# Kernel optimization log

Measured on AMD Instinct MI355X. Metric: run time of the kernel, lower is better.

## Reference

```python
import jax, jax.numpy as jnp
import numpy as np

EPS = 1e-6
STRIDES = (8, 16, 32)
IOU_THR = 0.5
GAMMA = 2.0
ALPHA = 1.0


def _ciou(b1, b2):
    # b1, b2: [..., 4] xywh boxes (broadcastable). Returns CIOU [...].
    b1xy, b1wh = b1[..., :2], b1[..., 2:]
    b2xy, b2wh = b2[..., :2], b2[..., 2:]
    b1lt, b1rb = b1xy - b1wh * 0.5, b1xy + b1wh * 0.5
    b2lt, b2rb = b2xy - b2wh * 0.5, b2xy + b2wh * 0.5
    lo1, hi1 = jnp.minimum(b1lt, b1rb), jnp.maximum(b1lt, b1rb)
    lo2, hi2 = jnp.minimum(b2lt, b2rb), jnp.maximum(b2lt, b2rb)
    area1 = (hi1[..., 0] - lo1[..., 0]) * (hi1[..., 1] - lo1[..., 1])
    area2 = (hi2[..., 0] - lo2[..., 0]) * (hi2[..., 1] - lo2[..., 1])
    iwh = jnp.clip(jnp.minimum(hi1, hi2) - jnp.maximum(lo1, lo2), 0.0, None)
    inter = iwh[..., 0] * iwh[..., 1]
    union = area1 + area2 - inter
    ious = inter / jnp.maximum(union, EPS)
    # smallest enclosing box diagonal
    owh = jnp.maximum(hi1, hi2) - jnp.minimum(lo1, lo2)
    c2 = jnp.maximum(owh[..., 0] ** 2 + owh[..., 1] ** 2, EPS)
    rho2 = jnp.sum((b1xy - b2xy) ** 2, axis=-1)
    u = rho2 / c2
    v = (4.0 / (np.pi ** 2)) * (
        jnp.arctan(b2wh[..., 0] / jnp.maximum(b2wh[..., 1], EPS))
        - jnp.arctan(b1wh[..., 0] / jnp.maximum(b1wh[..., 1], EPS))
    ) ** 2
    alpha = v / jnp.maximum(1.0 - ious + v, EPS)
    return ious - (u + alpha * v)


def _bce_logits(x, t):
    # stable BCEWithLogits, reduction='none'
    return jnp.logaddexp(0.0, x) - x * t


def _focal(x, t):
    return _bce_logits(x, t) * ALPHA * jnp.abs(t - jax.nn.sigmoid(x)) ** GAMMA


def _layer_loss(p, p_d, label, bboxes, stride):
    bs, grid = p.shape[0], p.shape[1]
    img_size = float(stride * grid)
    p_conf = p[..., 4:5]
    p_cls = p[..., 5:]
    p_d_xywh = p_d[..., :4]
    label_xywh = label[..., :4]
    obj = label[..., 4:5]
    mix = label[..., 5:6]
    label_cls = label[..., 6:]

    ciou = _ciou(p_d_xywh, label_xywh)[..., None]
    scale = 2.0 - label_xywh[..., 2:3] * label_xywh[..., 3:4] / (img_size ** 2)
    loss_ciou = obj * scale * (1.0 - ciou) * mix

    # pairwise CIOU between every pred box and up to 150 GT boxes: [bs,g,g,A,150]
    iou = _ciou(p_d_xywh[..., None, :], bboxes[:, None, None, None, :, :])
    iou_max = jnp.max(iou, axis=-1, keepdims=True)
    noobj = (1.0 - obj) * (iou_max < IOU_THR).astype(p.dtype)

    focal = _focal(p_conf, obj)
    loss_conf = (obj * focal + noobj * focal) * mix
    loss_cls = obj * _bce_logits(p_cls, label_cls) * mix

    l_ciou = jnp.sum(loss_ciou) / bs
    l_conf = jnp.sum(loss_conf) / bs
    l_cls = jnp.sum(loss_cls) / bs
    return l_ciou, l_conf, l_cls


def setup_inputs() -> dict:
    key = jax.random.key(0)
    B, A, NC, IMG = 4, 3, 20, 608
    grids = [76, 38, 19]
    inp = {}
    for i, g in enumerate(grids):
        k = jax.random.fold_in(key, i)
        ks = jax.random.split(k, 10)
        inp[f"p{i}"] = jax.random.normal(ks[0], (B, g, g, A, 5 + NC), jnp.float32)
        # decoded predictions: positive xywh in image coords + raw conf/cls
        xy = jax.random.uniform(ks[1], (B, g, g, A, 2)) * IMG
        wh = jax.random.uniform(ks[2], (B, g, g, A, 2)) * 120.0 + 2.0
        cc = jax.random.normal(ks[3], (B, g, g, A, 1 + NC))
        inp[f"p_d{i}"] = jnp.concatenate([xy, wh, cc], -1)
        # labels: xywh, obj (binary), mix (1.0), cls (binary)
        lxy = jax.random.uniform(ks[4], (B, g, g, A, 2)) * IMG
        lwh = jax.random.uniform(ks[5], (B, g, g, A, 2)) * 120.0 + 2.0
        obj = (jax.random.uniform(ks[6], (B, g, g, A, 1)) < 0.05).astype(jnp.float32)
        mix = jnp.ones((B, g, g, A, 1), jnp.float32)
        cls = (jax.random.uniform(ks[7], (B, g, g, A, NC)) < 0.5).astype(jnp.float32)
        inp[f"label{i}"] = jnp.concatenate([lxy, lwh, obj, mix, cls], -1)
        bxy = jax.random.uniform(ks[8], (B, 150, 2)) * IMG
        bwh = jax.random.uniform(ks[9], (B, 150, 2)) * 120.0 + 2.0
        inp[f"bboxes{i}"] = jnp.concatenate([bxy, bwh], -1)
    return inp


def reference(p0, p1, p2, p_d0, p_d1, p_d2, label0, label1, label2,
              bboxes0, bboxes1, bboxes2):
    ls_c, ls_conf, ls_cls = _layer_loss(p0, p_d0, label0, bboxes0, STRIDES[0])
    lm_c, lm_conf, lm_cls = _layer_loss(p1, p_d1, label1, bboxes1, STRIDES[1])
    ll_c, ll_conf, ll_cls = _layer_loss(p2, p_d2, label2, bboxes2, STRIDES[2])
    loss_ciou = ls_c + lm_c + ll_c
    loss_conf = ls_conf + lm_conf + ll_conf
    loss_cls = ls_cls + lm_cls + ll_cls
    loss = loss_ciou + loss_conf + loss_cls
    return (loss, loss_ciou, loss_conf, loss_cls)
```

## Files before the change

kernel.cpp:

```cpp
#include <hip/hip_runtime.h>
#include <math.h>

#define EPS   1e-6f
#define K_V   0.4052847345693511f
#define IMG2  369664.0f
#define NBOX  150
#define NBOXP 152
#define NCLS  20

#define BPB_L0 271
#define BPB_L1 68
#define BPB_L2 17
#define NBLK   (4*(BPB_L0+BPB_L1+BPB_L2))

__device__ __forceinline__ float fast_rcp(float x) { return __builtin_amdgcn_rcpf(x); }

__device__ __forceinline__ float bce_logits(float x, float t) {
    float e = __expf(-fabsf(x));
    return fmaxf(x, 0.f) + __logf(1.f + e) - x * t;
}

__device__ __forceinline__ float wave_sum(float v) {
#pragma unroll
    for (int off = 32; off > 0; off >>= 1) v += __shfl_down(v, off, 64);
    return v;
}

__global__ __launch_bounds__(256, 6) void yolo_loss_kernel(
    const float* __restrict__ p0,  const float* __restrict__ pd0,
    const float* __restrict__ lb0, const float* __restrict__ bb0,
    const float* __restrict__ p1,  const float* __restrict__ pd1,
    const float* __restrict__ lb1, const float* __restrict__ bb1,
    const float* __restrict__ p2,  const float* __restrict__ pd2,
    const float* __restrict__ lb2, const float* __restrict__ bb2,
    float* __restrict__ ws, float* __restrict__ out)
{
    __shared__ float4 s_box[NBOXP];
    __shared__ float4 s_aux[NBOXP];
    __shared__ float  s_part[4][3];

    const int blk = blockIdx.x;
    const float *p, *pd, *lb, *bb;
    int batch, lblk, apb;
    if (blk < 4*BPB_L0) {
        p = p0; pd = pd0; lb = lb0; bb = bb0;
        batch = blk / BPB_L0; lblk = blk % BPB_L0; apb = 17328;
    } else if (blk < 4*(BPB_L0+BPB_L1)) {
        int r = blk - 4*BPB_L0;
        p = p1; pd = pd1; lb = lb1; bb = bb1;
        batch = r / BPB_L1; lblk = r % BPB_L1; apb = 4332;
    } else {
        int r = blk - 4*(BPB_L0+BPB_L1);
        p = p2; pd = pd2; lb = lb2; bb = bb2;
        batch = r / BPB_L2; lblk = r % BPB_L2; apb = 1083;
    }

    const int tid  = threadIdx.x;
    const int wave = tid >> 6, lane = tid & 63;
    const int q = lane >> 4, s = lane & 15;
    const int a = lblk * 64 + wave * 16 + s;
    const bool active = (a < apb);
    const size_t base = (size_t)batch * apb + a;
    const float* lbp = lb + base * 26;

    float b1x = 0.f, b1y = 0.f, b1w = 1.f, b1h = 1.f;
    float obj = 0.f, mix = 0.f, pconf = 0.f;
    if (active) {
        const float* pdp = pd + base * 25;
        b1x = pdp[0]; b1y = pdp[1]; b1w = pdp[2]; b1h = pdp[3];
        float2 om = *(const float2*)(lbp + 4);
        obj = om.x; mix = om.y;
        pconf = p[base * 25 + 4];
    }

    if (tid < NBOXP) {
        float bx, by, bw, bh;
        if (tid < NBOX) {
            float4 b = ((const float4*)bb)[batch * NBOX + tid];
            bx = b.x; by = b.y; bw = b.z; bh = b.w;
        } else {
            bx = 3.0e30f; by = 3.0e30f; bw = 0.f; bh = 1.f;
        }
        float hw = bw * 0.5f, hh = bh * 0.5f;
        float ltx = bx - hw, lty = by - hh, rbx = bx + hw, rby = by + hh;
        float lox = fminf(ltx, rbx), hix = fmaxf(ltx, rbx);
        float loy = fminf(lty, rby), hiy = fmaxf(lty, rby);
        s_box[tid] = make_float4(lox, loy, hix, hiy);
        s_aux[tid] = make_float4((hix - lox) * (hiy - loy), bx, by,
                                 atanf(bw / fmaxf(bh, EPS)));
    }
    __syncthreads();

    float lo1x = 0.f, lo1y = 0.f, hi1x = 0.f, hi1y = 0.f, area1 = 0.f;
    {
        const float hw = b1w * 0.5f, hh = b1h * 0.5f;
        const float l1x = b1x - hw, l1y = b1y - hh;
        const float r1x = b1x + hw, r1y = b1y + hh;
        lo1x = fminf(l1x, r1x); hi1x = fmaxf(l1x, r1x);
        lo1y = fminf(l1y, r1y); hi1y = fmaxf(l1y, r1y);
        area1 = (hi1x - lo1x) * (hi1y - lo1y);
    }

    const int j0 = q * 38;
    unsigned long long mask = 0ull;
    if (active && obj == 0.f) {
#pragma unroll 4
        for (int k = 0; k < 38; ++k) {
            float4 b4 = s_box[j0 + k];
            float a2  = s_aux[j0 + k].x;
            float ix0 = fmaxf(lo1x, b4.x), iy0 = fmaxf(lo1y, b4.y);
            float ix1 = fminf(hi1x, b4.z), iy1 = fminf(hi1y, b4.w);
            float iwx = fmaxf(ix1 - ix0, 0.f);
            float iwy = fmaxf(iy1 - iy0, 0.f);
            float inter = iwx * iwy;
            float uni_m = fmaxf(area1 + a2 - inter, EPS);
            float metric = fmaf(-0.999996f, uni_m, inter + inter);
            mask |= (unsigned long long)(metric > 0.f) << k;
        }
    }

    int hit = 0;
    if (mask) {
        const float at1 = atanf(b1w / fmaxf(b1h, EPS));
        unsigned long long m = mask;
        do {
            int k = __ffsll(m) - 1; m &= m - 1;
            float4 b4 = s_box[j0 + k];
            float4 ax = s_aux[j0 + k];
            float ix0 = fmaxf(lo1x, b4.x), iy0 = fmaxf(lo1y, b4.y);
            float ix1 = fminf(hi1x, b4.z), iy1 = fminf(hi1y, b4.w);
            float iwx = fmaxf(ix1 - ix0, 0.f);
            float iwy = fmaxf(iy1 - iy0, 0.f);
            float inter = iwx * iwy;
            float iou = inter * fast_rcp(fmaxf(area1 + ax.x - inter, EPS));
            float owx = fmaxf(hi1x, b4.z) - fminf(lo1x, b4.x);
            float owy = fmaxf(hi1y, b4.w) - fminf(lo1y, b4.y);
            float c2 = fmaxf(owx * owx + owy * owy, EPS);
            float dx = b1x - ax.y, dy = b1y - ax.z;
            float u = (dx * dx + dy * dy) * fast_rcp(c2);
            float dv = ax.w - at1;
            float v = K_V * dv * dv;
            float alpha = v * fast_rcp(fmaxf(1.f - iou + v, EPS));
            float ci = iou - (u + alpha * v);
            hit |= (ci >= 0.5f);
        } while (m);
    }
    hit |= __shfl_xor(hit, 16, 64);
    hit |= __shfl_xor(hit, 32, 64);

    float t_ciou = 0.f, t_conf = 0.f, t_cls = 0.f;
    if (active && q == 0) {
        const float sig = fast_rcp(1.f + __expf(-pconf));
        const float dd = fabsf(obj - sig);
        const float focal = bce_logits(pconf, obj) * (dd * dd);
        float gate;
        if (obj > 0.f) {
            const float at1 = atanf(b1w / fmaxf(b1h, EPS));
            float2 lxy = *(const float2*)(lbp + 0);
            float2 lwh = *(const float2*)(lbp + 2);
            const float lx = lxy.x, ly = lxy.y, lw = lwh.x, lh = lwh.y;
            const float hlw = lw * 0.5f, hlh = lh * 0.5f;
            const float l2x = lx - hlw, l2y = ly - hlh;
            const float r2x = lx + hlw, r2y = ly + hlh;
            const float lo2x = fminf(l2x, r2x), hi2x = fmaxf(l2x, r2x);
            const float lo2y = fminf(l2y, r2y), hi2y = fmaxf(l2y, r2y);
            const float area2 = (hi2x - lo2x) * (hi2y - lo2y);
            float iwx = fmaxf(fminf(hi1x, hi2x) - fmaxf(lo1x, lo2x), 0.f);
            float iwy = fmaxf(fminf(hi1y, hi2y) - fmaxf(lo1y, lo2y), 0.f);
            float inter = iwx * iwy;
            float iou = inter * fast_rcp(fmaxf(area1 + area2 - inter, EPS));
            float owx = fmaxf(hi1x, hi2x) - fminf(lo1x, lo2x);
            float owy = fmaxf(hi1y, hi2y) - fminf(lo1y, lo2y);
            float c2 = fmaxf(owx * owx + owy * owy, EPS);
            float dx = b1x - lx, dy = b1y - ly;
            float u = (dx * dx + dy * dy) * fast_rcp(c2);
            float at2 = atanf(lw / fmaxf(lh, EPS));
            float dv = at2 - at1;
            float v = K_V * dv * dv;
            float alpha = v * fast_rcp(fmaxf(1.f - iou + v, EPS));
            float ciou = iou - (u + alpha * v);

            float scale = 2.f - lw * lh * (1.f / IMG2);
            t_ciou = scale * (1.f - ciou) * mix;

            float cs = 0.f;
            const float* pc = p + base * 25 + 5;
            const float* lc = lbp + 6;
#pragma unroll
            for (int c = 0; c < NCLS; ++c) cs += bce_logits(pc[c], lc[c]);
            t_cls = cs * mix;
            gate = 1.f;
        } else {
            gate = hit ? 0.f : 1.f;
        }
        t_conf = gate * focal * mix;
    }

    float r0 = wave_sum(t_ciou);
    float r1 = wave_sum(t_conf);
    float r2 = wave_sum(t_cls);
    if (lane == 0) { s_part[wave][0] = r0; s_part[wave][1] = r1; s_part[wave][2] = r2; }
    __syncthreads();

    if (tid == 0) {
        float c = 0.f, f = 0.f, cl = 0.f;
#pragma unroll
        for (int w = 0; w < 4; ++w) { c += s_part[w][0]; f += s_part[w][1]; cl += s_part[w][2]; }
        const int slot = (blk & 7) * 16;
        atomicAdd(&ws[slot + 0], c);
        atomicAdd(&ws[slot + 1], f);
        atomicAdd(&ws[slot + 2], cl);
        __threadfence();
        unsigned old = atomicAdd((unsigned*)(ws + 128), 1u);
        if (old == NBLK - 1) {
            __threadfence();
            float C = 0.f, F = 0.f, CL = 0.f;
#pragma unroll
            for (int sl = 0; sl < 8; ++sl) {
                C  += atomicAdd(&ws[sl*16 + 0], 0.f);
                F  += atomicAdd(&ws[sl*16 + 1], 0.f);
                CL += atomicAdd(&ws[sl*16 + 2], 0.f);
            }
            const float inv_bs = 0.25f;
            out[0] = (C + F + CL) * inv_bs;
            out[1] = C * inv_bs;
            out[2] = F * inv_bs;
            out[3] = CL * inv_bs;
        }
    }
}

extern "C" void kernel_launch(void* const* d_in, const int* in_sizes, int n_in,
                              void* d_out, int out_size, void* d_ws, size_t ws_size,
                              hipStream_t stream) {
    const float* p0  = (const float*)d_in[0];
    const float* pd0 = (const float*)d_in[1];
    const float* lb0 = (const float*)d_in[2];
    const float* bb0 = (const float*)d_in[3];
    const float* p1  = (const float*)d_in[4];
    const float* pd1 = (const float*)d_in[5];
    const float* lb1 = (const float*)d_in[6];
    const float* bb1 = (const float*)d_in[7];
    const float* p2  = (const float*)d_in[8];
    const float* pd2 = (const float*)d_in[9];
    const float* lb2 = (const float*)d_in[10];
    const float* bb2 = (const float*)d_in[11];

    float* ws = (float*)d_ws;
    hipMemsetAsync(ws, 0, 132 * sizeof(float), stream);

    yolo_loss_kernel<<<NBLK, 256, 0, stream>>>(
        p0, pd0, lb0, bb0, p1, pd1, lb1, bb1, p2, pd2, lb2, bb2,
        ws, (float*)d_out);
}
```

Baseline: 124.9 us.

## Stage per-block anchor rows in LDS with coalesced loads; split class BCE across quads

Each block now loads its 64 anchors' p, p_d and label rows into shared memory with fully coalesced strided loads, replacing the scattered per-thread strided global reads. The later stages read box, obj, conf and label fields from LDS. The 20-class BCE sum is spread over the four quad lanes, five classes each, instead of being done serially by one lane. This adds about 20KB of LDS per block, which may lower occupancy under launch_bounds(256,6), and it loads the full rows even though most anchors only need a few fields.

Result: slower. 127.7 us (+2.2%).

```diff
diff --git a/kernel.cpp b/kernel.cpp
--- a/kernel.cpp
+++ b/kernel.cpp
@@ -12,6 +12,9 @@
 #define BPB_L1 68
 #define BPB_L2 17
 #define NBLK   (4*(BPB_L0+BPB_L1+BPB_L2))
+
+#define NDW_P  1600
+#define NDW_LB 1664
 
 __device__ __forceinline__ float fast_rcp(float x) { return __builtin_amdgcn_rcpf(x); }
 
@@ -35,6 +38,7 @@
     const float* __restrict__ lb2, const float* __restrict__ bb2,
     float* __restrict__ ws, float* __restrict__ out)
 {
+    __shared__ float  s_pd[NDW_P], s_lb[NDW_LB], s_p[NDW_P];
     __shared__ float4 s_box[NBOXP];
     __shared__ float4 s_aux[NBOXP];
     __shared__ float  s_part[4][3];
@@ -55,55 +59,66 @@
         batch = r / BPB_L2; lblk = r % BPB_L2; apb = 1083;
     }
 
-    const int tid  = threadIdx.x;
-    const int wave = tid >> 6, lane = tid & 63;
-    const int q = lane >> 4, s = lane & 15;
-    const int a = lblk * 64 + wave * 16 + s;
-    const bool active = (a < apb);
-    const size_t base = (size_t)batch * apb + a;
-    const float* lbp = lb + base * 26;
-
-    float b1x = 0.f, b1y = 0.f, b1w = 1.f, b1h = 1.f;
-    float obj = 0.f, mix = 0.f, pconf = 0.f;
-    if (active) {
-        const float* pdp = pd + base * 25;
-        b1x = pdp[0]; b1y = pdp[1]; b1w = pdp[2]; b1h = pdp[3];
-        float2 om = *(const float2*)(lbp + 4);
-        obj = om.x; mix = om.y;
-        pconf = p[base * 25 + 4];
-    }
+    const int tid = threadIdx.x;
+    const int navail = min(64, apb - lblk * 64);
+    const size_t base0 = (size_t)batch * apb + (size_t)lblk * 64;
+
+    const float* gpd = pd + base0 * 25;
+    const float* glb = lb + base0 * 26;
+    const float* gp  = p  + base0 * 25;
+    const int ndw_p  = navail * 25;
+    const int ndw_lb = navail * 26;
+
+    float vpd[7], vlb[7], vp[7];
+#pragma unroll
+    for (int i = 0; i < 7; ++i) { int idx = tid + i*256; vpd[i] = (idx < ndw_p)  ? gpd[idx] : 0.f; }
+#pragma unroll
+    for (int i = 0; i < 7; ++i) { int idx = tid + i*256; vlb[i] = (idx < ndw_lb) ? glb[idx] : 0.f; }
+#pragma unroll
+    for (int i = 0; i < 7; ++i) { int idx = tid + i*256; vp[i]  = (idx < ndw_p)  ? gp[idx]  : 0.f; }
+
+    float4 bxy = make_float4(3.0e30f, 3.0e30f, 0.f, 1.f);
+    if (tid < NBOX) bxy = ((const float4*)bb)[batch * NBOX + tid];
+
+#pragma unroll
+    for (int i = 0; i < 7; ++i) { int idx = tid + i*256; if (idx < NDW_P)  s_pd[idx] = vpd[i]; }
+#pragma unroll
+    for (int i = 0; i < 7; ++i) { int idx = tid + i*256; if (idx < NDW_LB) s_lb[idx] = vlb[i]; }
+#pragma unroll
+    for (int i = 0; i < 7; ++i) { int idx = tid + i*256; if (idx < NDW_P)  s_p[idx]  = vp[i]; }
 
     if (tid < NBOXP) {
-        float bx, by, bw, bh;
-        if (tid < NBOX) {
-            float4 b = ((const float4*)bb)[batch * NBOX + tid];
-            bx = b.x; by = b.y; bw = b.z; bh = b.w;
-        } else {
-            bx = 3.0e30f; by = 3.0e30f; bw = 0.f; bh = 1.f;
-        }
-        float hw = bw * 0.5f, hh = bh * 0.5f;
-        float ltx = bx - hw, lty = by - hh, rbx = bx + hw, rby = by + hh;
+        float hw = bxy.z * 0.5f, hh = bxy.w * 0.5f;
+        float ltx = bxy.x - hw, lty = bxy.y - hh, rbx = bxy.x + hw, rby = bxy.y + hh;
         float lox = fminf(ltx, rbx), hix = fmaxf(ltx, rbx);
         float loy = fminf(lty, rby), hiy = fmaxf(lty, rby);
         s_box[tid] = make_float4(lox, loy, hix, hiy);
-        s_aux[tid] = make_float4((hix - lox) * (hiy - loy), bx, by,
-                                 atanf(bw / fmaxf(bh, EPS)));
+        s_aux[tid] = make_float4((hix - lox) * (hiy - loy), bxy.x, bxy.y,
+                                 atanf(bxy.z / fmaxf(bxy.w, EPS)));
     }
     __syncthreads();
 
-    float lo1x = 0.f, lo1y = 0.f, hi1x = 0.f, hi1y = 0.f, area1 = 0.f;
-    {
-        const float hw = b1w * 0.5f, hh = b1h * 0.5f;
-        const float l1x = b1x - hw, l1y = b1y - hh;
-        const float r1x = b1x + hw, r1y = b1y + hh;
-        lo1x = fminf(l1x, r1x); hi1x = fmaxf(l1x, r1x);
-        lo1y = fminf(l1y, r1y); hi1y = fmaxf(l1y, r1y);
-        area1 = (hi1x - lo1x) * (hi1y - lo1y);
-    }
+    const int wave = tid >> 6, lane = tid & 63;
+    const int q = lane >> 4, s = lane & 15;
+    const int row = wave * 16 + s;
+    const bool active = (row < navail);
+    const size_t base = base0 + row;
+
+    const float b1x = s_pd[row*25 + 0], b1y = s_pd[row*25 + 1];
+    const float b1w = s_pd[row*25 + 2], b1h = s_pd[row*25 + 3];
+    const float obj = s_lb[row*26 + 4], mix = s_lb[row*26 + 5];
+    const float pconf = s_p[row*25 + 4];
+
+    const float hw = b1w * 0.5f, hh = b1h * 0.5f;
+    const float l1x = b1x - hw, l1y = b1y - hh;
+    const float r1x = b1x + hw, r1y = b1y + hh;
+    const float lo1x = fminf(l1x, r1x), hi1x = fmaxf(l1x, r1x);
+    const float lo1y = fminf(l1y, r1y), hi1y = fmaxf(l1y, r1y);
+    const float area1 = (hi1x - lo1x) * (hi1y - lo1y);
 
     const int j0 = q * 38;
     unsigned long long mask = 0ull;
-    if (active && obj == 0.f) {
+    if (obj == 0.f) {
 #pragma unroll 4
         for (int k = 0; k < 38; ++k) {
             float4 b4 = s_box[j0 + k];
@@ -149,6 +164,15 @@
     hit |= __shfl_xor(hit, 32, 64);
 
     float t_ciou = 0.f, t_conf = 0.f, t_cls = 0.f;
+    if (active && obj > 0.f) {
+        float cs = 0.f;
+#pragma unroll
+        for (int c = 0; c < 5; ++c) {
+            int cc = q * 5 + c;
+            cs += bce_logits(s_p[row*25 + 5 + cc], s_lb[row*26 + 6 + cc]);
+        }
+        t_cls = cs * mix;
+    }
     if (active && q == 0) {
         const float sig = fast_rcp(1.f + __expf(-pconf));
         const float dd = fabsf(obj - sig);
@@ -156,9 +180,8 @@
         float gate;
         if (obj > 0.f) {
             const float at1 = atanf(b1w / fmaxf(b1h, EPS));
-            float2 lxy = *(const float2*)(lbp + 0);
-            float2 lwh = *(const float2*)(lbp + 2);
-            const float lx = lxy.x, ly = lxy.y, lw = lwh.x, lh = lwh.y;
+            const float lx = s_lb[row*26 + 0], ly = s_lb[row*26 + 1];
+            const float lw = s_lb[row*26 + 2], lh = s_lb[row*26 + 3];
             const float hlw = lw * 0.5f, hlh = lh * 0.5f;
             const float l2x = lx - hlw, l2y = ly - hlh;
             const float r2x = lx + hlw, r2y = ly + hlh;
@@ -182,13 +205,6 @@
 
             float scale = 2.f - lw * lh * (1.f / IMG2);
             t_ciou = scale * (1.f - ciou) * mix;
-
-            float cs = 0.f;
-            const float* pc = p + base * 25 + 5;
-            const float* lc = lbp + 6;
-#pragma unroll
-            for (int c = 0; c < NCLS; ++c) cs += bce_logits(pc[c], lc[c]);
-            t_cls = cs * mix;
             gate = 1.f;
         } else {
             gate = hit ? 0.f : 1.f;
```

## Split GT-box scan across 8 lanes per anchor and spread class BCE

Applied to the files above, without the earlier changes.

Each anchor is now handled by 8 lanes, each scanning 19 of the 152 GT boxes, instead of 4 lanes scanning 38. Blocks therefore cover 32 anchors instead of 64, and the grid doubles. The class BCE loop for positive anchors is spread over those lanes. Box loads are hoisted ahead of shared-memory setup, out-of-range anchors use clamped unconditional loads, and the box area in the prefilter is recomputed from s_box rather than read from s_aux. Occupancy is also raised to 8 blocks per SIMD. The intent is shorter serial chains per thread and more latency hiding, at the cost of more blocks and redundant per-anchor loads across lanes.

New measurement: 161.5 us. +29.3%, slower.

```diff
diff --git a/kernel.cpp b/kernel.cpp
--- a/kernel.cpp
+++ b/kernel.cpp
@@ -8,10 +8,13 @@
 #define NBOXP 152
 #define NCLS  20
 
-#define BPB_L0 271
-#define BPB_L1 68
-#define BPB_L2 17
-#define NBLK   (4*(BPB_L0+BPB_L1+BPB_L2))
+#define APB0  17328
+#define APB1  4332
+#define APB2  1083
+#define BPB_L0 542
+#define BPB_L1 136
+#define BPB_L2 34
+#define NBLK  (4*(BPB_L0+BPB_L1+BPB_L2))
 
 __device__ __forceinline__ float fast_rcp(float x) { return __builtin_amdgcn_rcpf(x); }
 
@@ -26,7 +29,7 @@
     return v;
 }
 
-__global__ __launch_bounds__(256, 6) void yolo_loss_kernel(
+__global__ __launch_bounds__(256, 8) void yolo_loss_kernel(
     const float* __restrict__ p0,  const float* __restrict__ pd0,
     const float* __restrict__ lb0, const float* __restrict__ bb0,
     const float* __restrict__ p1,  const float* __restrict__ pd1,
@@ -44,70 +47,61 @@
     int batch, lblk, apb;
     if (blk < 4*BPB_L0) {
         p = p0; pd = pd0; lb = lb0; bb = bb0;
-        batch = blk / BPB_L0; lblk = blk % BPB_L0; apb = 17328;
+        batch = blk / BPB_L0; lblk = blk % BPB_L0; apb = APB0;
     } else if (blk < 4*(BPB_L0+BPB_L1)) {
         int r = blk - 4*BPB_L0;
         p = p1; pd = pd1; lb = lb1; bb = bb1;
-        batch = r / BPB_L1; lblk = r % BPB_L1; apb = 4332;
+        batch = r / BPB_L1; lblk = r % BPB_L1; apb = APB1;
     } else {
         int r = blk - 4*(BPB_L0+BPB_L1);
         p = p2; pd = pd2; lb = lb2; bb = bb2;
-        batch = r / BPB_L2; lblk = r % BPB_L2; apb = 1083;
+        batch = r / BPB_L2; lblk = r % BPB_L2; apb = APB2;
     }
 
     const int tid  = threadIdx.x;
     const int wave = tid >> 6, lane = tid & 63;
-    const int q = lane >> 4, s = lane & 15;
-    const int a = lblk * 64 + wave * 16 + s;
-    const bool active = (a < apb);
-    const size_t base = (size_t)batch * apb + a;
+    const int o = lane >> 3, s = lane & 7;
+    const int arow = lblk * 32 + wave * 8 + s;
+    const bool active = (arow < apb);
+    const int rowc = min(arow, apb - 1);
+    const size_t base = (size_t)batch * apb + rowc;
+
+    float4 bxy = make_float4(3.0e30f, 3.0e30f, 0.f, 1.f);
+    if (tid < NBOX) bxy = ((const float4*)bb)[batch * NBOX + tid];
+
+    const float* pdp = pd + base * 25;
     const float* lbp = lb + base * 26;
-
-    float b1x = 0.f, b1y = 0.f, b1w = 1.f, b1h = 1.f;
-    float obj = 0.f, mix = 0.f, pconf = 0.f;
-    if (active) {
-        const float* pdp = pd + base * 25;
-        b1x = pdp[0]; b1y = pdp[1]; b1w = pdp[2]; b1h = pdp[3];
-        float2 om = *(const float2*)(lbp + 4);
-        obj = om.x; mix = om.y;
-        pconf = p[base * 25 + 4];
-    }
+    const float b1x = pdp[0], b1y = pdp[1], b1w = pdp[2], b1h = pdp[3];
+    const float2 om = *(const float2*)(lbp + 4);
+    const float obj = om.x, mix = om.y;
+    const float pconf = p[base * 25 + 4];
 
     if (tid < NBOXP) {
-        float bx, by, bw, bh;
-        if (tid < NBOX) {
-            float4 b = ((const float4*)bb)[batch * NBOX + tid];
-            bx = b.x; by = b.y; bw = b.z; bh = b.w;
-        } else {
-            bx = 3.0e30f; by = 3.0e30f; bw = 0.f; bh = 1.f;
-        }
-        float hw = bw * 0.5f, hh = bh * 0.5f;
-        float ltx = bx - hw, lty = by - hh, rbx = bx + hw, rby = by + hh;
+        float hw = bxy.z * 0.5f, hh = bxy.w * 0.5f;
+        float ltx = bxy.x - hw, lty = bxy.y - hh;
+        float rbx = bxy.x + hw, rby = bxy.y + hh;
         float lox = fminf(ltx, rbx), hix = fmaxf(ltx, rbx);
         float loy = fminf(lty, rby), hiy = fmaxf(lty, rby);
         s_box[tid] = make_float4(lox, loy, hix, hiy);
-        s_aux[tid] = make_float4((hix - lox) * (hiy - loy), bx, by,
-                                 atanf(bw / fmaxf(bh, EPS)));
+        s_aux[tid] = make_float4((hix - lox) * (hiy - loy), bxy.x, bxy.y,
+                                 atanf(bxy.z / fmaxf(bxy.w, EPS)));
     }
     __syncthreads();
 
-    float lo1x = 0.f, lo1y = 0.f, hi1x = 0.f, hi1y = 0.f, area1 = 0.f;
-    {
-        const float hw = b1w * 0.5f, hh = b1h * 0.5f;
-        const float l1x = b1x - hw, l1y = b1y - hh;
-        const float r1x = b1x + hw, r1y = b1y + hh;
-        lo1x = fminf(l1x, r1x); hi1x = fmaxf(l1x, r1x);
-        lo1y = fminf(l1y, r1y); hi1y = fmaxf(l1y, r1y);
-        area1 = (hi1x - lo1x) * (hi1y - lo1y);
-    }
-
-    const int j0 = q * 38;
-    unsigned long long mask = 0ull;
-    if (active && obj == 0.f) {
-#pragma unroll 4
-        for (int k = 0; k < 38; ++k) {
+    const float hw = b1w * 0.5f, hh = b1h * 0.5f;
+    const float l1x = b1x - hw, l1y = b1y - hh;
+    const float r1x = b1x + hw, r1y = b1y + hh;
+    const float lo1x = fminf(l1x, r1x), hi1x = fmaxf(l1x, r1x);
+    const float lo1y = fminf(l1y, r1y), hi1y = fmaxf(l1y, r1y);
+    const float area1 = (hi1x - lo1x) * (hi1y - lo1y);
+
+    const int j0 = o * 19;
+    unsigned mask = 0u;
+    if (obj == 0.f) {
+#pragma unroll
+        for (int k = 0; k < 19; ++k) {
             float4 b4 = s_box[j0 + k];
-            float a2  = s_aux[j0 + k].x;
+            float a2  = (b4.z - b4.x) * (b4.w - b4.y);
             float ix0 = fmaxf(lo1x, b4.x), iy0 = fmaxf(lo1y, b4.y);
             float ix1 = fminf(hi1x, b4.z), iy1 = fminf(hi1y, b4.w);
             float iwx = fmaxf(ix1 - ix0, 0.f);
@@ -115,16 +109,16 @@
             float inter = iwx * iwy;
             float uni_m = fmaxf(area1 + a2 - inter, EPS);
             float metric = fmaf(-0.999996f, uni_m, inter + inter);
-            mask |= (unsigned long long)(metric > 0.f) << k;
+            mask |= (unsigned)(metric > 0.f) << k;
         }
     }
 
     int hit = 0;
     if (mask) {
         const float at1 = atanf(b1w / fmaxf(b1h, EPS));
-        unsigned long long m = mask;
+        unsigned m = mask;
         do {
-            int k = __ffsll(m) - 1; m &= m - 1;
+            int k = __ffs(m) - 1; m &= m - 1;
             float4 b4 = s_box[j0 + k];
             float4 ax = s_aux[j0 + k];
             float ix0 = fmaxf(lo1x, b4.x), iy0 = fmaxf(lo1y, b4.y);
@@ -145,19 +139,27 @@
             hit |= (ci >= 0.5f);
         } while (m);
     }
+    hit |= __shfl_xor(hit, 8, 64);
     hit |= __shfl_xor(hit, 16, 64);
     hit |= __shfl_xor(hit, 32, 64);
 
     float t_ciou = 0.f, t_conf = 0.f, t_cls = 0.f;
-    if (active && q == 0) {
+    if (active && obj > 0.f) {
+        float cs = 0.f;
+        const float* pc = p + base * 25 + 5;
+        const float* lc = lbp + 6;
+        for (int c = o; c < NCLS; c += 8) cs += bce_logits(pc[c], lc[c]);
+        t_cls = cs * mix;
+    }
+    if (active && o == 0) {
         const float sig = fast_rcp(1.f + __expf(-pconf));
         const float dd = fabsf(obj - sig);
         const float focal = bce_logits(pconf, obj) * (dd * dd);
         float gate;
         if (obj > 0.f) {
             const float at1 = atanf(b1w / fmaxf(b1h, EPS));
-            float2 lxy = *(const float2*)(lbp + 0);
-            float2 lwh = *(const float2*)(lbp + 2);
+            const float2 lxy = *(const float2*)(lbp + 0);
+            const float2 lwh = *(const float2*)(lbp + 2);
             const float lx = lxy.x, ly = lxy.y, lw = lwh.x, lh = lwh.y;
             const float hlw = lw * 0.5f, hlh = lh * 0.5f;
             const float l2x = lx - hlw, l2y = ly - hlh;
@@ -179,16 +181,8 @@
             float v = K_V * dv * dv;
             float alpha = v * fast_rcp(fmaxf(1.f - iou + v, EPS));
             float ciou = iou - (u + alpha * v);
-
             float scale = 2.f - lw * lh * (1.f / IMG2);
             t_ciou = scale * (1.f - ciou) * mix;
-
-            float cs = 0.f;
-            const float* pc = p + base * 25 + 5;
-            const float* lc = lbp + 6;
-#pragma unroll
-            for (int c = 0; c < NCLS; ++c) cs += bce_logits(pc[c], lc[c]);
-            t_cls = cs * mix;
             gate = 1.f;
         } else {
             gate = hit ? 0.f : 1.f;
```
